# Optimization experiments

Hardware: AMD Instinct MI355X
Metric: run time of the kernel (lower is better)

The kernel has to match this reference:

```python
import jax, jax.numpy as jnp
import numpy as np

N_SEND = 49152   # 12 * 64^2 HEALPix nodes
N_REC = 65536    # 256x256 receiver grid
N_EDGES = 262144 # N_REC * 4 nearest senders
D_MODEL = 256
EDGE_IN, EDGE_OUT = 4, 64
LIN_IN, LIN_OUT = 320, 256
B = 2


def setup_inputs() -> dict:
    key = jax.random.key(0)
    ks = jax.random.split(key, 8)
    x = jax.random.normal(ks[0], (B, N_SEND, D_MODEL), dtype=jnp.float32)
    senders = jax.random.randint(ks[1], (N_EDGES,), 0, N_SEND, dtype=jnp.int32)
    receivers = jax.random.randint(ks[2], (N_EDGES,), 0, N_REC, dtype=jnp.int32)
    edge_index = jnp.stack([senders, receivers], axis=0)
    edge_attr = jax.random.normal(ks[3], (N_EDGES, EDGE_IN), dtype=jnp.float32)
    s = lambda fan_in: 1.0 / np.sqrt(fan_in)
    return {
        "x": x,
        "edge_index": edge_index,
        "edge_attr": edge_attr,
        "ee_w1": jax.random.normal(ks[4], (EDGE_IN, EDGE_OUT), dtype=jnp.float32) * s(EDGE_IN),
        "ee_b1": jnp.zeros((EDGE_OUT,), dtype=jnp.float32),
        "ee_w2": jax.random.normal(ks[5], (EDGE_OUT, EDGE_OUT), dtype=jnp.float32) * s(EDGE_OUT),
        "ee_b2": jnp.zeros((EDGE_OUT,), dtype=jnp.float32),
        "ff_w1": jax.random.normal(ks[6], (LIN_IN, LIN_OUT), dtype=jnp.float32) * s(LIN_IN),
        "ff_b1": jnp.zeros((LIN_OUT,), dtype=jnp.float32),
        "ff_w2": jax.random.normal(ks[7], (LIN_OUT, LIN_OUT), dtype=jnp.float32) * s(LIN_OUT),
        "ff_b2": jnp.zeros((LIN_OUT,), dtype=jnp.float32),
    }


def reference(x, edge_index, edge_attr,
              ee_w1, ee_b1, ee_w2, ee_b2,
              ff_w1, ff_b1, ff_w2, ff_b2):
    senders, receivers = edge_index[0], edge_index[1]
    # edge embedder MLP: [E, edge_in] -> [E, edge_out]
    h = jax.nn.relu(edge_attr @ ee_w1 + ee_b1)
    edge_feat = h @ ee_w2 + ee_b2                       # [E, edge_out]
    # gather sender node features: [B, E, d_model]
    v_s = x[:, senders, :]
    # concat with broadcast edge features: [B, E, d_model + edge_out]
    ef = jnp.broadcast_to(edge_feat[None], (x.shape[0],) + edge_feat.shape)
    v_s_prime = jnp.concatenate([v_s, ef], axis=-1)
    # scatter-sum onto receiver nodes: [B, n_rec, lin_in]
    v_m_sum = jnp.zeros((x.shape[0], N_REC, v_s_prime.shape[-1]), dtype=x.dtype)
    v_m_sum = v_m_sum.at[:, receivers, :].add(v_s_prime)
    # g2m feedforward: [B, n_rec, lin_out]
    h2 = jax.nn.relu(v_m_sum @ ff_w1 + ff_b1)
    return h2 @ ff_w2 + ff_b2
```

## Files before the change

### kernel.cpp

```cpp
#include <hip/hip_runtime.h>
#include <hip/hip_bf16.h>

#define N_SEND 49152
#define N_REC  65536
#define N_EDGES 262144
#define D_MODEL 256
#define EDGE_IN 4
#define EDGE_OUT 64
#define LIN_IN 320
#define LIN_OUT 256
#define BATCH 2

#define EPB 32
#define GBM 128

typedef __attribute__((ext_vector_type(4))) float f32x4;
typedef __attribute__((ext_vector_type(8))) short bf16x8;

static __device__ __forceinline__ unsigned short f2bf(float f) {
    union { float f; unsigned u; } v; v.f = f;
    unsigned r = v.u + 0x7FFF + ((v.u >> 16) & 1);
    return (unsigned short)(r >> 16);
}
static __device__ __forceinline__ float bf2f(unsigned short h) {
    union { unsigned u; float f; } v; v.u = ((unsigned)h) << 16; return v.f;
}

static __device__ __forceinline__ void async_copy16(void* lds_ptr, const void* g_ptr) {
    __builtin_amdgcn_global_load_lds(
        (const __attribute__((address_space(1))) void*)g_ptr,
        (__attribute__((address_space(3))) void*)lds_ptr, 16, 0, 0);
}

__global__ __launch_bounds__(256) void prep_fused(
    const float* __restrict__ x, unsigned short* __restrict__ xb, int nconv,
    const int* __restrict__ receivers, const float* __restrict__ edge_attr,
    const float* __restrict__ ee_w1, const float* __restrict__ ee_b1,
    const float* __restrict__ ee_w2, const float* __restrict__ ee_b2,
    unsigned short* __restrict__ efs, int* __restrict__ counts,
    const float* __restrict__ w1, const float* __restrict__ w2,
    unsigned short* __restrict__ w1t, unsigned short* __restrict__ w2t)
{
    __shared__ float h_lds[EPB][EDGE_OUT];
    __shared__ float e_lds[EPB][EDGE_OUT];

    const int bid = blockIdx.x;
    const int tid = threadIdx.x;

    if (bid < nconv) {
        const size_t i = ((size_t)bid * 256 + tid) * 8;
        const float4 v0 = *(const float4*)&x[i];
        const float4 v1 = *(const float4*)&x[i + 4];
        bf16x8 o;
        o[0] = (short)f2bf(v0.x); o[1] = (short)f2bf(v0.y);
        o[2] = (short)f2bf(v0.z); o[3] = (short)f2bf(v0.w);
        o[4] = (short)f2bf(v1.x); o[5] = (short)f2bf(v1.y);
        o[6] = (short)f2bf(v1.z); o[7] = (short)f2bf(v1.w);
        *(bf16x8*)&xb[i] = o;
        return;
    }
    const int b2 = bid - nconv;

    if (b2 < N_EDGES / EPB) {
        const int e0 = b2 * EPB;

        if (tid < EPB) atomicAdd(&counts[receivers[e0 + tid]], 1);

        for (int i = tid; i < EPB * EDGE_OUT; i += 256) {
            const int e = i >> 6, j = i & 63;
            const float* ea = edge_attr + (size_t)(e0 + e) * EDGE_IN;
            float acc = ee_b1[j];
            acc += ea[0] * ee_w1[0 * EDGE_OUT + j];
            acc += ea[1] * ee_w1[1 * EDGE_OUT + j];
            acc += ea[2] * ee_w1[2 * EDGE_OUT + j];
            acc += ea[3] * ee_w1[3 * EDGE_OUT + j];
            h_lds[e][j] = fmaxf(acc, 0.0f);
        }
        __syncthreads();

        {
            const int j = tid & 63, g = tid >> 6;
            float acc[8];
#pragma unroll
            for (int e = 0; e < 8; ++e) acc[e] = ee_b2[j];
            for (int k = 0; k < EDGE_OUT; ++k) {
                const float w = ee_w2[k * EDGE_OUT + j];
#pragma unroll
                for (int e = 0; e < 8; ++e) acc[e] += h_lds[g * 8 + e][k] * w;
            }
#pragma unroll
            for (int e = 0; e < 8; ++e) e_lds[g * 8 + e][j] = acc[e];
        }
        __syncthreads();

        {
            const int e = tid >> 3, seg = tid & 7;
            const float* src = &e_lds[e][seg * 8];
            bf16x8 o;
#pragma unroll
            for (int j = 0; j < 8; ++j) o[j] = (short)f2bf(src[j]);
            *(bf16x8*)&efs[(size_t)(e0 + e) * EDGE_OUT + seg * 8] = o;
        }
        return;
    }

    {
        const int t3 = (b2 - N_EDGES / EPB) * 256 + tid;
        if (t3 < 256 * LIN_IN) {
            const int n = t3 / LIN_IN, k = t3 - n * LIN_IN;
            w1t[t3] = f2bf(w1[k * LIN_OUT + n]);
        } else {
            const int t2 = t3 - 256 * LIN_IN;
            if (t2 < 256 * 256) {
                const int n = t2 >> 8, k = t2 & 255;
                w2t[t2] = f2bf(w2[k * LIN_OUT + n]);
            }
        }
    }
}

__global__ __launch_bounds__(1024) void scan_kernel(
    const int* __restrict__ counts, int* __restrict__ row_ptr,
    int* __restrict__ cursor)
{
    __shared__ int sums[1024];
    const int t = threadIdx.x;
    const int4* c4 = (const int4*)(counts + t * 64);

    int s = 0;
#pragma unroll
    for (int i = 0; i < 16; ++i) { const int4 c = c4[i]; s += c.x + c.y + c.z + c.w; }
    sums[t] = s;
    __syncthreads();

    for (int off = 1; off < 1024; off <<= 1) {
        const int v = (t >= off) ? sums[t - off] : 0;
        __syncthreads();
        sums[t] += v;
        __syncthreads();
    }

    int run = sums[t] - s;
#pragma unroll
    for (int i = 0; i < 16; ++i) {
        const int4 c = c4[i];
        int4 w;
        w.x = run; w.y = run + c.x; w.z = w.y + c.y; w.w = w.z + c.z;
        run = w.w + c.w;
        ((int4*)(row_ptr + t * 64))[i] = w;
        ((int4*)(cursor + t * 64))[i] = w;
    }
    if (t == 1023) row_ptr[N_REC] = run;
}

__global__ __launch_bounds__(256) void fill_kernel(
    const int* __restrict__ senders, const int* __restrict__ receivers,
    int* __restrict__ cursor, int* __restrict__ edge_order,
    int* __restrict__ ssort)
{
    const int e = blockIdx.x * 256 + threadIdx.x;
    const int r = receivers[e];
    const int pos = atomicAdd(&cursor[r], 1);
    edge_order[pos] = e;
    ssort[pos] = senders[e];
}

template<bool XB>
__global__ __launch_bounds__(256) void gather_kernel(
    const float* __restrict__ x,
    const unsigned short* __restrict__ xb,
    const unsigned short* __restrict__ efs,
    const int* __restrict__ row_ptr,
    const int* __restrict__ edge_order,
    const int* __restrict__ ssort,
    unsigned short* __restrict__ vmb)
{
    const int lane = threadIdx.x & 63;
    const int wave = threadIdx.x >> 6;
    const int r = blockIdx.x * 4 + wave;
    const int beg = row_ptr[r], end = row_ptr[r + 1];
    const int half = lane >> 5, l2 = lane & 31;

    float ax[8] = {0, 0, 0, 0, 0, 0, 0, 0};
    float ae[8] = {0, 0, 0, 0, 0, 0, 0, 0};

    for (int chunk = beg; chunk < end; chunk += 64) {
        const int n = min(64, end - chunk);
        int myidx = 0, myeidx = 0;
        if (chunk + lane < end) {
            myidx = ssort[chunk + lane];
            myeidx = edge_order[chunk + lane];
        }
        for (int i = 0; i < n; ++i) {
            const int s = __shfl(myidx, i);
            const int e = __shfl(myeidx, i);
            const size_t rowbase = (size_t)(half ? N_SEND + s : s) * D_MODEL;
            if (XB) {
                const bf16x8 v = *(const bf16x8*)&xb[rowbase + l2 * 8];
#pragma unroll
                for (int j = 0; j < 8; ++j) ax[j] += bf2f((unsigned short)v[j]);
            } else {
                const float4 v0 = *(const float4*)&x[rowbase + l2 * 8];
                const float4 v1 = *(const float4*)&x[rowbase + l2 * 8 + 4];
                ax[0] += v0.x; ax[1] += v0.y; ax[2] += v0.z; ax[3] += v0.w;
                ax[4] += v1.x; ax[5] += v1.y; ax[6] += v1.z; ax[7] += v1.w;
            }
            if (lane < 8) {
                const bf16x8 w = *(const bf16x8*)&efs[(size_t)e * EDGE_OUT + lane * 8];
#pragma unroll
                for (int j = 0; j < 8; ++j) ae[j] += bf2f((unsigned short)w[j]);
            }
        }
    }

    bf16x8 o;
#pragma unroll
    for (int j = 0; j < 8; ++j) o[j] = (short)f2bf(ax[j]);
    *(bf16x8*)&vmb[((size_t)(half * N_REC + r)) * LIN_IN + l2 * 8] = o;
    if (lane < 8) {
        bf16x8 oe;
#pragma unroll
        for (int j = 0; j < 8; ++j) oe[j] = (short)f2bf(ae[j]);
        *(bf16x8*)&vmb[((size_t)r) * LIN_IN + D_MODEL + lane * 8] = oe;
        *(bf16x8*)&vmb[((size_t)(N_REC + r)) * LIN_IN + D_MODEL + lane * 8] = oe;
    }
}

__global__ __launch_bounds__(512, 1) void node_mlp_fused(
    const unsigned short* __restrict__ vmb,
    const unsigned short* __restrict__ w1t,
    const float* __restrict__ b1,
    const unsigned short* __restrict__ w2t,
    const float* __restrict__ b2,
    float* __restrict__ out)
{
    __shared__ __align__(16) char lds[114688];

    const int tid  = threadIdx.x;
    const int lane = tid & 63, wave = tid >> 6;
    const int n16  = lane & 15, hi = lane >> 4;
    const int wr   = wave >> 2, wc = wave & 3;
    const size_t row0 = (size_t)blockIdx.x * GBM;
    char* const hbase = lds + 49152;

    const int f_l = (n16 & 3) ^ ((n16 >> 2) & 3);
    const int hsl = (hi ^ f_l) << 4;

    auto stageA = [&](int kk, int buf) {
        const int row = tid >> 2;
        const int sl = (tid & 3) ^ ((row & 3) ^ ((row >> 2) & 3));
        const unsigned short* g = vmb + (row0 + row) * LIN_IN + kk + sl * 8;
        char* l = lds + (buf << 13) + ((tid >> 6) << 10);
        async_copy16(l, g);
    };
    auto stageB = [&](const unsigned short* BT, int ldk, int kk, int buf) {
#pragma unroll
        for (int p = 0; p < 2; ++p) {
            const int i = p * 512 + tid, row = i >> 2;
            const int sl = (i & 3) ^ ((row & 3) ^ ((row >> 2) & 3));
            const unsigned short* g = BT + (size_t)row * ldk + kk + sl * 8;
            char* l = lds + 16384 + (buf << 14) + (p << 13) + ((tid >> 6) << 10);
            async_copy16(l, g);
        }
    };

    f32x4 acc[4][4];
#pragma unroll
    for (int c = 0; c < 4; ++c) {
        const float bv = b1[64 * wc + 16 * c + n16];
#pragma unroll
        for (int t = 0; t < 4; ++t) {
            acc[t][c][0] = bv; acc[t][c][1] = bv; acc[t][c][2] = bv; acc[t][c][3] = bv;
        }
    }

    stageA(0, 0); stageB(w1t, LIN_IN, 0, 0);
    int cur = 0;
    for (int step = 0; step < LIN_IN / 32; ++step) {
        if (step + 1 < LIN_IN / 32) {
            stageA((step + 1) * 32, cur ^ 1);
            stageB(w1t, LIN_IN, (step + 1) * 32, cur ^ 1);
        }
        __syncthreads();

        bf16x8 af[4], bf[4];
        const char* Ab = lds + (cur << 13);
        const char* Bb = lds + 16384 + (cur << 14);
#pragma unroll
        for (int t = 0; t < 4; ++t)
            af[t] = *(const bf16x8*)(Ab + (64 * wr + 16 * t + n16) * 64 + hsl);
#pragma unroll
        for (int c = 0; c < 4; ++c)
            bf[c] = *(const bf16x8*)(Bb + (64 * wc + 16 * c + n16) * 64 + hsl);
#pragma unroll
        for (int c = 0; c < 4; ++c)
#pragma unroll
            for (int t = 0; t < 4; ++t)
                acc[t][c] = __builtin_amdgcn_mfma_f32_16x16x32_bf16(af[t], bf[c], acc[t][c], 0, 0, 0);

        __syncthreads();
        cur ^= 1;
    }

#pragma unroll
    for (int t = 0; t < 4; ++t)
#pragma unroll
        for (int c = 0; c < 4; ++c) {
            const int col = 64 * wc + 16 * c + n16;
            const int kc = col >> 5;
            const int b  = (col & 31) * 2;
            const int gslot = b >> 4;
#pragma unroll
            for (int r = 0; r < 4; ++r) {
                const int lrow = 64 * wr + 16 * t + 4 * hi + r;
                const int f = (lrow & 3) ^ ((lrow >> 2) & 3);
                *(unsigned short*)(hbase + (kc << 13) + lrow * 64 + (((gslot ^ f) << 4) | (b & 15))) =
                    f2bf(fmaxf(acc[t][c][r], 0.0f));
            }
        }
    __syncthreads();

    f32x4 acc2[4][4];
#pragma unroll
    for (int c = 0; c < 4; ++c) {
        const float bv = b2[64 * wc + 16 * c + n16];
#pragma unroll
        for (int t = 0; t < 4; ++t) {
            acc2[t][c][0] = bv; acc2[t][c][1] = bv; acc2[t][c][2] = bv; acc2[t][c][3] = bv;
        }
    }

    stageB(w2t, LIN_OUT, 0, 0);
    cur = 0;
    for (int step = 0; step < LIN_OUT / 32; ++step) {
        if (step + 1 < LIN_OUT / 32) stageB(w2t, LIN_OUT, (step + 1) * 32, cur ^ 1);
        __syncthreads();

        bf16x8 af[4], bf[4];
        const char* Hb = hbase + (step << 13);
        const char* Bb = lds + 16384 + (cur << 14);
#pragma unroll
        for (int t = 0; t < 4; ++t)
            af[t] = *(const bf16x8*)(Hb + (64 * wr + 16 * t + n16) * 64 + hsl);
#pragma unroll
        for (int c = 0; c < 4; ++c)
            bf[c] = *(const bf16x8*)(Bb + (64 * wc + 16 * c + n16) * 64 + hsl);
#pragma unroll
        for (int c = 0; c < 4; ++c)
#pragma unroll
            for (int t = 0; t < 4; ++t)
                acc2[t][c] = __builtin_amdgcn_mfma_f32_16x16x32_bf16(af[t], bf[c], acc2[t][c], 0, 0, 0);

        __syncthreads();
        cur ^= 1;
    }

#pragma unroll
    for (int t = 0; t < 4; ++t)
#pragma unroll
        for (int c = 0; c < 4; ++c)
#pragma unroll
            for (int r = 0; r < 4; ++r)
                out[(row0 + 64 * wr + 16 * t + 4 * hi + r) * LIN_OUT + 64 * wc + 16 * c + n16] =
                    acc2[t][c][r];
}

extern "C" void kernel_launch(void* const* d_in, const int* in_sizes, int n_in,
                              void* d_out, int out_size, void* d_ws, size_t ws_size,
                              hipStream_t stream) {
    const float* x         = (const float*)d_in[0];
    const int*   edge_idx  = (const int*)d_in[1];
    const float* edge_attr = (const float*)d_in[2];
    const float* ee_w1     = (const float*)d_in[3];
    const float* ee_b1     = (const float*)d_in[4];
    const float* ee_w2     = (const float*)d_in[5];
    const float* ee_b2     = (const float*)d_in[6];
    const float* ff_w1     = (const float*)d_in[7];
    const float* ff_b1     = (const float*)d_in[8];
    const float* ff_w2     = (const float*)d_in[9];
    const float* ff_b2     = (const float*)d_in[10];
    float* out = (float*)d_out;

    const int* senders   = edge_idx;
    const int* receivers = edge_idx + N_EDGES;

    char* ws = (char*)d_ws;
    size_t off = 0;
    auto alloc = [&](size_t bytes) { char* p = ws + off; off += (bytes + 511) & ~511ull; return p; };

    unsigned short* vmb = (unsigned short*)alloc((size_t)BATCH * N_REC * LIN_IN * 2);
    unsigned short* efs = (unsigned short*)alloc((size_t)N_EDGES * EDGE_OUT * 2);
    unsigned short* w1t = (unsigned short*)alloc((size_t)256 * LIN_IN * 2);
    unsigned short* w2t = (unsigned short*)alloc((size_t)256 * LIN_OUT * 2);
    int* row_ptr        = (int*)alloc((size_t)(N_REC + 1) * 4);
    int* counts         = (int*)alloc((size_t)N_REC * 4);
    int* cursor         = (int*)alloc((size_t)N_REC * 4);
    int* edge_order     = (int*)alloc((size_t)N_EDGES * 4);
    int* ssort          = (int*)alloc((size_t)N_EDGES * 4);
    const size_t base_need = off;
    unsigned short* xb  = (unsigned short*)(ws + off);
    const size_t xb_bytes = (size_t)BATCH * N_SEND * D_MODEL * 2;
    const bool use_xb = (ws_size >= base_need + xb_bytes);

    hipMemsetAsync(counts, 0, (size_t)N_REC * 4, stream);

    const int nconv = use_xb ? (int)((size_t)BATCH * N_SEND * D_MODEL / 8 / 256) : 0;
    const int prep_grid = nconv + N_EDGES / EPB + (256 * LIN_IN + 256 * LIN_OUT + 255) / 256;
    prep_fused<<<prep_grid, 256, 0, stream>>>(
        x, xb, nconv, receivers, edge_attr, ee_w1, ee_b1, ee_w2, ee_b2,
        efs, counts, ff_w1, ff_w2, w1t, w2t);

    scan_kernel<<<1, 1024, 0, stream>>>(counts, row_ptr, cursor);

    fill_kernel<<<N_EDGES / 256, 256, 0, stream>>>(
        senders, receivers, cursor, edge_order, ssort);

    if (use_xb) {
        gather_kernel<true><<<N_REC / 4, 256, 0, stream>>>(
            x, xb, efs, row_ptr, edge_order, ssort, vmb);
    } else {
        gather_kernel<false><<<N_REC / 4, 256, 0, stream>>>(
            x, xb, efs, row_ptr, edge_order, ssort, vmb);
    }

    node_mlp_fused<<<(BATCH * N_REC) / GBM, 512, 0, stream>>>(
        vmb, w1t, ff_b1, w2t, ff_b2, out);
}
```

Before: 285.2 us.

## Compute edge-embedder second layer with bf16 MFMA over 256-edge blocks

The edge-embedder MLP in the prep kernel now handles 256 edges per block (one per thread) instead of 32. Each thread computes its hidden row, converts it to bf16 and stores it into an XOR-swizzled LDS tile. The 64x64 second layer then runs as 16x16x32 bf16 MFMA per wave, replacing the scalar FP32 loop and its two block barriers. In exchange, the hidden activations and ee_w2 are rounded to bf16 before the matmul, and the output is written with scattered 2-byte stores instead of 16-byte vector stores.

```diff
diff --git a/kernel.cpp b/kernel.cpp
--- a/kernel.cpp
+++ b/kernel.cpp
@@ -11,7 +11,6 @@
 #define LIN_OUT 256
 #define BATCH 2
 
-#define EPB 32
 #define GBM 128
 
 typedef __attribute__((ext_vector_type(4))) float f32x4;
@@ -41,8 +40,7 @@
     const float* __restrict__ w1, const float* __restrict__ w2,
     unsigned short* __restrict__ w1t, unsigned short* __restrict__ w2t)
 {
-    __shared__ float h_lds[EPB][EDGE_OUT];
-    __shared__ float e_lds[EPB][EDGE_OUT];
+    __shared__ __align__(16) unsigned short h_lds[256 * EDGE_OUT];
 
     const int bid = blockIdx.x;
     const int tid = threadIdx.x;
@@ -61,51 +59,86 @@
     }
     const int b2 = bid - nconv;
 
-    if (b2 < N_EDGES / EPB) {
-        const int e0 = b2 * EPB;
-
-        if (tid < EPB) atomicAdd(&counts[receivers[e0 + tid]], 1);
-
-        for (int i = tid; i < EPB * EDGE_OUT; i += 256) {
-            const int e = i >> 6, j = i & 63;
-            const float* ea = edge_attr + (size_t)(e0 + e) * EDGE_IN;
-            float acc = ee_b1[j];
-            acc += ea[0] * ee_w1[0 * EDGE_OUT + j];
-            acc += ea[1] * ee_w1[1 * EDGE_OUT + j];
-            acc += ea[2] * ee_w1[2 * EDGE_OUT + j];
-            acc += ea[3] * ee_w1[3 * EDGE_OUT + j];
-            h_lds[e][j] = fmaxf(acc, 0.0f);
-        }
-        __syncthreads();
+    if (b2 < N_EDGES / 256) {
+        const int e0 = b2 * 256;
+        atomicAdd(&counts[receivers[e0 + tid]], 1);
 
         {
-            const int j = tid & 63, g = tid >> 6;
-            float acc[8];
-#pragma unroll
-            for (int e = 0; e < 8; ++e) acc[e] = ee_b2[j];
-            for (int k = 0; k < EDGE_OUT; ++k) {
-                const float w = ee_w2[k * EDGE_OUT + j];
-#pragma unroll
-                for (int e = 0; e < 8; ++e) acc[e] += h_lds[g * 8 + e][k] * w;
-            }
-#pragma unroll
-            for (int e = 0; e < 8; ++e) e_lds[g * 8 + e][j] = acc[e];
-        }
-        __syncthreads();
-
-        {
-            const int e = tid >> 3, seg = tid & 7;
-            const float* src = &e_lds[e][seg * 8];
-            bf16x8 o;
-#pragma unroll
-            for (int j = 0; j < 8; ++j) o[j] = (short)f2bf(src[j]);
-            *(bf16x8*)&efs[(size_t)(e0 + e) * EDGE_OUT + seg * 8] = o;
-        }
+            const float4 ea = *(const float4*)&edge_attr[(size_t)(e0 + tid) * EDGE_IN];
+#pragma unroll
+            for (int kb = 0; kb < 8; ++kb) {
+                bf16x8 hv;
+#pragma unroll
+                for (int j = 0; j < 8; ++j) {
+                    const int k = kb * 8 + j;
+                    float a = ee_b1[k];
+                    a += ea.x * ee_w1[0 * EDGE_OUT + k];
+                    a += ea.y * ee_w1[1 * EDGE_OUT + k];
+                    a += ea.z * ee_w1[2 * EDGE_OUT + k];
+                    a += ea.w * ee_w1[3 * EDGE_OUT + k];
+                    hv[j] = (short)f2bf(fmaxf(a, 0.0f));
+                }
+                h_lds[tid * EDGE_OUT + ((kb ^ (tid & 7)) * 8)] = 0;
+                *(bf16x8*)&h_lds[tid * EDGE_OUT + ((kb ^ (tid & 7)) * 8)] = hv;
+            }
+        }
+
+        const int lane = tid & 63, wave = tid >> 6;
+        const int n16 = lane & 15, hi = lane >> 4;
+
+        bf16x8 bfr[2][4];
+#pragma unroll
+        for (int ch = 0; ch < 2; ++ch)
+#pragma unroll
+            for (int c = 0; c < 4; ++c) {
+                bf16x8 b;
+#pragma unroll
+                for (int j = 0; j < 8; ++j) {
+                    const int k = ch * 32 + hi * 8 + j;
+                    b[j] = (short)f2bf(ee_w2[k * EDGE_OUT + 16 * c + n16]);
+                }
+                bfr[ch][c] = b;
+            }
+
+        f32x4 acc[4][4];
+#pragma unroll
+        for (int c = 0; c < 4; ++c) {
+            const float bv = ee_b2[16 * c + n16];
+#pragma unroll
+            for (int t = 0; t < 4; ++t) {
+                acc[t][c][0] = bv; acc[t][c][1] = bv; acc[t][c][2] = bv; acc[t][c][3] = bv;
+            }
+        }
+
+#pragma unroll
+        for (int ch = 0; ch < 2; ++ch) {
+            bf16x8 af[4];
+#pragma unroll
+            for (int t = 0; t < 4; ++t) {
+                const int row = 64 * wave + 16 * t + n16;
+                const int slot = (4 * ch + hi) ^ (row & 7);
+                af[t] = *(const bf16x8*)&h_lds[row * EDGE_OUT + slot * 8];
+            }
+#pragma unroll
+            for (int c = 0; c < 4; ++c)
+#pragma unroll
+                for (int t = 0; t < 4; ++t)
+                    acc[t][c] = __builtin_amdgcn_mfma_f32_16x16x32_bf16(af[t], bfr[ch][c], acc[t][c], 0, 0, 0);
+        }
+
+#pragma unroll
+        for (int t = 0; t < 4; ++t)
+#pragma unroll
+            for (int c = 0; c < 4; ++c)
+#pragma unroll
+                for (int r = 0; r < 4; ++r)
+                    efs[(size_t)(e0 + 64 * wave + 16 * t + 4 * hi + r) * EDGE_OUT + 16 * c + n16] =
+                        f2bf(acc[t][c][r]);
         return;
     }
 
     {
-        const int t3 = (b2 - N_EDGES / EPB) * 256 + tid;
+        const int t3 = (b2 - N_EDGES / 256) * 256 + tid;
         if (t3 < 256 * LIN_IN) {
             const int n = t3 / LIN_IN, k = t3 - n * LIN_IN;
             w1t[t3] = f2bf(w1[k * LIN_OUT + n]);
@@ -405,7 +438,7 @@
     hipMemsetAsync(counts, 0, (size_t)N_REC * 4, stream);
 
     const int nconv = use_xb ? (int)((size_t)BATCH * N_SEND * D_MODEL / 8 / 256) : 0;
-    const int prep_grid = nconv + N_EDGES / EPB + (256 * LIN_IN + 256 * LIN_OUT + 255) / 256;
+    const int prep_grid = nconv + N_EDGES / 256 + (256 * LIN_IN + 256 * LIN_OUT + 255) / 256;
     prep_fused<<<prep_grid, 256, 0, stream>>>(
         x, xb, nconv, receivers, edge_attr, ee_w1, ee_b1, ee_w2, ee_b2,
         efs, counts, ff_w1, ff_w2, w1t, w2t);
```

After: 252.0 us. -11.6%, faster.
